# Performance work log

Measured on AMD Instinct MI355X. Metric: run time of the kernel, lower is better.

## Reference

```python
import math
import jax, jax.numpy as jnp
import numpy as np

B, S, D, H = 2, 2048, 1024, 16
HD = D // H  # head_dim = 64


def setup_inputs() -> dict:
    key = jax.random.key(0)
    k1, k2, k3 = jax.random.split(key, 3)
    scale = 0.02
    return {
        "x": jax.random.normal(k1, (B, S, D), dtype=jnp.float32),
        "w_qkv": jax.random.normal(k2, (D, 3 * D), dtype=jnp.float32) * scale,
        "b_qkv": jnp.zeros((3 * D,), dtype=jnp.float32),
        "w_proj": jax.random.normal(k3, (D, D), dtype=jnp.float32) * scale,
        "b_proj": jnp.zeros((D,), dtype=jnp.float32),
    }


def reference(x, w_qkv, b_qkv, w_proj, b_proj):
    bsz, seq_len, d_model = x.shape
    # fused qkv projection: [B,S,3D] -> [3,B,H,S,HD]
    qkv = (x @ w_qkv + b_qkv).reshape(bsz, seq_len, 3, H, HD)
    qkv = jnp.transpose(qkv, (2, 0, 3, 1, 4))
    q, k, v = qkv[0], qkv[1], qkv[2]
    # scores [B,H,S,S]
    scores = jnp.einsum("bhqd,bhkd->bhqk", q, k) / math.sqrt(HD)
    causal = jnp.tril(jnp.ones((seq_len, seq_len), dtype=bool))
    scores = jnp.where(causal[None, None], scores, -jnp.inf)
    probs = jax.nn.softmax(scores, axis=-1)
    # dropout = 0.0 (eval mode)
    context = jnp.einsum("bhqk,bhkd->bhqd", probs, v)
    context = jnp.transpose(context, (0, 2, 1, 3)).reshape(bsz, seq_len, d_model)
    return context @ w_proj + b_proj
```

## Files before the change

kernel.cpp:

```cpp
#include <hip/hip_runtime.h>

#define B_ 2
#define S_ 2048
#define D_ 1024
#define H_ 16
#define HD_ 64
#define M_ (B_*S_)
#define N_QKV (3*D_)

typedef __attribute__((ext_vector_type(8))) short short8;
typedef __attribute__((ext_vector_type(4))) float floatx4;

__device__ __forceinline__ float fast_exp2(float x) {
    return __builtin_amdgcn_exp2f(x);
}

__device__ __forceinline__ unsigned short f2b(float f) {
    union { float f; unsigned int u; } v; v.f = f;
    unsigned int u = v.u;
    u += 0x7FFFu + ((u >> 16) & 1u);
    return (unsigned short)(u >> 16);
}
__device__ __forceinline__ unsigned short f2b_fast(float f) {
    union { float f; unsigned int u; } v; v.f = f;
    return (unsigned short)((v.u + 0x8000u) >> 16);
}

__device__ __forceinline__ void glds16(const unsigned short* g, unsigned short* lds) {
    __builtin_amdgcn_global_load_lds(
        (const __attribute__((address_space(1))) unsigned int*)g,
        (__attribute__((address_space(3))) unsigned int*)lds, 16, 0, 0);
}

__global__ void cast_bf16_kernel(const float* __restrict__ src,
                                 unsigned short* __restrict__ dst, int n) {
    int i = (blockIdx.x * blockDim.x + threadIdx.x) * 4;
    if (i >= n) return;
    float4 f = *(const float4*)(src + i);
    ushort4 o;
    o.x = f2b(f.x); o.y = f2b(f.y); o.z = f2b(f.z); o.w = f2b(f.w);
    *(ushort4*)(dst + i) = o;
}

__global__ void transpose_cast_kernel(const float* __restrict__ W,
                                      unsigned short* __restrict__ Wt,
                                      int rows, int cols) {
    __shared__ float tile[32][33];
    int c0 = blockIdx.x * 32, r0 = blockIdx.y * 32;
    int tx = threadIdx.x, ty = threadIdx.y;
    #pragma unroll
    for (int i = 0; i < 4; ++i)
        tile[ty + i*8][tx] = W[(size_t)(r0 + ty + i*8) * cols + c0 + tx];
    __syncthreads();
    #pragma unroll
    for (int i = 0; i < 4; ++i)
        Wt[(size_t)(c0 + ty + i*8) * rows + r0 + tx] = f2b(tile[tx][ty + i*8]);
}

__global__ __launch_bounds__(256, 3) void gemm_bt_kernel(
    const unsigned short* __restrict__ A,
    const unsigned short* __restrict__ Bt,
    const float* __restrict__ bias,
    unsigned short* __restrict__ q,
    unsigned short* __restrict__ k_,
    unsigned short* __restrict__ vt,
    int Kdim)
{
    __shared__ unsigned short SMEM[128*136];
    unsigned short* As = SMEM;
    unsigned short* Bs = SMEM + 128*64;

    const int t = threadIdx.x;
    const int lane = t & 63;
    const int w = t >> 6;
    const int wm = w >> 1, wn = w & 1;
    const int quad = lane >> 4, l15 = lane & 15;
    const int bm = blockIdx.y, bn = blockIdx.x;

    const int sr32 = t >> 3;
    const int gch  = (t & 7) ^ (sr32 & 7);

    const unsigned short* gA = A  + (size_t)(bm*128 + sr32) * Kdim + gch*8;
    const unsigned short* gB = Bt + (size_t)(bn*128 + sr32) * Kdim + gch*8;
    const size_t rstep = (size_t)32 * Kdim;

    unsigned short* lA = As + (w*8)*64;
    unsigned short* lB = Bs + (w*8)*64;

    const int swz = (l15 & 7);

    auto stage_g = [&](int kk) {
        #pragma unroll
        for (int c = 0; c < 4; ++c) {
            glds16(gA + c*rstep + kk, lA + c*2048);
            glds16(gB + c*rstep + kk, lB + c*2048);
        }
    };

    floatx4 acc[4][4];
    #pragma unroll
    for (int i = 0; i < 4; ++i)
        #pragma unroll
        for (int j = 0; j < 4; ++j)
            acc[i][j] = (floatx4){0.f, 0.f, 0.f, 0.f};

    stage_g(0);
    for (int k0 = 0; k0 < Kdim; k0 += 64) {
        __syncthreads();
        short8 an[4][2], am[4][2];
        #pragma unroll
        for (int i = 0; i < 4; ++i)
            #pragma unroll
            for (int kk = 0; kk < 2; ++kk) {
                const int coff = ((quad + 4*kk) ^ swz) * 8;
                an[i][kk] = *(const short8*)&Bs[(wn*64 + i*16 + l15)*64 + coff];
                am[i][kk] = *(const short8*)&As[(wm*64 + i*16 + l15)*64 + coff];
            }
        __syncthreads();
        if (k0 + 64 < Kdim) stage_g(k0 + 64);
        #pragma unroll
        for (int kk = 0; kk < 2; ++kk)
            #pragma unroll
            for (int i = 0; i < 4; ++i)
                #pragma unroll
                for (int j = 0; j < 4; ++j)
                    acc[i][j] = __builtin_amdgcn_mfma_f32_16x16x32_bf16(an[i][kk], am[j][kk], acc[i][j], 0, 0, 0);
    }

    const float QSCALE = 0.18033688011112042f;
    const int which = bn >> 3;
    const int hcol  = (bn & 7)*2 + wn;
    const int b     = bm >> 4;
    const int sbase0 = (bm & 15)*128;
    const int sbase  = sbase0 + wm*64;

    if (which == 2) {
        unsigned short (*L)[136] = (unsigned short (*)[136])SMEM;
        #pragma unroll
        for (int i = 0; i < 4; ++i) {
            float4 bias4 = *(const float4*)&bias[bn*128 + wn*64 + i*16 + quad*4];
            const int n0 = wn*64 + i*16 + quad*4;
            #pragma unroll
            for (int j = 0; j < 4; ++j) {
                const int m = wm*64 + j*16 + l15;
                L[n0+0][m] = f2b(acc[i][j][0] + bias4.x);
                L[n0+1][m] = f2b(acc[i][j][1] + bias4.y);
                L[n0+2][m] = f2b(acc[i][j][2] + bias4.z);
                L[n0+3][m] = f2b(acc[i][j][3] + bias4.w);
            }
        }
        __syncthreads();
        const int r = t >> 1, half = t & 1;
        const int hcr = (bn & 7)*2 + (r >> 6);
        const int hdr = r & 63;
        unsigned short* dst = &vt[(((size_t)(b*H_ + hcr))*HD_ + hdr)*S_ + sbase0 + half*64];
        const unsigned short* srcL = &L[r][half*64];
        #pragma unroll
        for (int c = 0; c < 8; ++c)
            *(uint4*)&dst[c*8] = *(const uint4*)&srcL[c*8];
    } else {
        #pragma unroll
        for (int i = 0; i < 4; ++i) {
            float4 bias4 = *(const float4*)&bias[bn*128 + wn*64 + i*16 + quad*4];
            const int hd0 = i*16 + quad*4;
            #pragma unroll
            for (int j = 0; j < 4; ++j) {
                const int srow = sbase + j*16 + l15;
                float v0 = acc[i][j][0] + bias4.x;
                float v1 = acc[i][j][1] + bias4.y;
                float v2 = acc[i][j][2] + bias4.z;
                float v3 = acc[i][j][3] + bias4.w;
                if (which == 0) {
                    v0 *= QSCALE; v1 *= QSCALE; v2 *= QSCALE; v3 *= QSCALE;
                    ushort4 o; o.x = f2b(v0); o.y = f2b(v1); o.z = f2b(v2); o.w = f2b(v3);
                    *(ushort4*)&q[((size_t)(b*H_ + hcol) * S_ + srow) * HD_ + hd0] = o;
                } else {
                    ushort4 o; o.x = f2b(v0); o.y = f2b(v1); o.z = f2b(v2); o.w = f2b(v3);
                    *(ushort4*)&k_[((size_t)(b*H_ + hcol) * S_ + srow) * HD_ + hd0] = o;
                }
            }
        }
    }
}

__global__ __launch_bounds__(256, 2) void gemm_bt64_kernel(
    const unsigned short* __restrict__ A,
    const unsigned short* __restrict__ Bt,
    const float* __restrict__ bias,
    float* __restrict__ outf,
    int Ndim, int Kdim)
{
    __shared__ unsigned short As[128*64];
    __shared__ unsigned short Bs[64*64];

    const int t = threadIdx.x;
    const int lane = t & 63;
    const int w = t >> 6;
    const int quad = lane >> 4, l15 = lane & 15;
    const int bm = blockIdx.y, bn = blockIdx.x;

    const int sr32 = t >> 3;
    const int gch  = (t & 7) ^ (sr32 & 7);

    const unsigned short* gA = A  + (size_t)(bm*128 + sr32) * Kdim + gch*8;
    const unsigned short* gB = Bt + (size_t)(bn*64  + sr32) * Kdim + gch*8;
    const size_t rstep = (size_t)32 * Kdim;

    unsigned short* lA = As + (w*8)*64;
    unsigned short* lB = Bs + (w*8)*64;

    const int swz = (l15 & 7);

    auto stage_g = [&](int kk) {
        #pragma unroll
        for (int c = 0; c < 4; ++c)
            glds16(gA + c*rstep + kk, lA + c*2048);
        #pragma unroll
        for (int c = 0; c < 2; ++c)
            glds16(gB + c*rstep + kk, lB + c*2048);
    };

    floatx4 acc[4][2];
    #pragma unroll
    for (int i = 0; i < 4; ++i)
        #pragma unroll
        for (int j = 0; j < 2; ++j)
            acc[i][j] = (floatx4){0.f, 0.f, 0.f, 0.f};

    stage_g(0);
    for (int k0 = 0; k0 < Kdim; k0 += 64) {
        __syncthreads();
        short8 an[4][2], am[2][2];
        #pragma unroll
        for (int kk = 0; kk < 2; ++kk) {
            const int coff = ((quad + 4*kk) ^ swz) * 8;
            #pragma unroll
            for (int i = 0; i < 4; ++i)
                an[i][kk] = *(const short8*)&Bs[(i*16 + l15)*64 + coff];
            #pragma unroll
            for (int j = 0; j < 2; ++j)
                am[j][kk] = *(const short8*)&As[(w*32 + j*16 + l15)*64 + coff];
        }
        __syncthreads();
        if (k0 + 64 < Kdim) stage_g(k0 + 64);
        #pragma unroll
        for (int kk = 0; kk < 2; ++kk)
            #pragma unroll
            for (int i = 0; i < 4; ++i)
                #pragma unroll
                for (int j = 0; j < 2; ++j)
                    acc[i][j] = __builtin_amdgcn_mfma_f32_16x16x32_bf16(an[i][kk], am[j][kk], acc[i][j], 0, 0, 0);
    }

    #pragma unroll
    for (int i = 0; i < 4; ++i) {
        float4 bias4 = *(const float4*)&bias[bn*64 + i*16 + quad*4];
        #pragma unroll
        for (int j = 0; j < 2; ++j) {
            const int gm = bm*128 + w*32 + j*16 + l15;
            float4 o;
            o.x = acc[i][j][0] + bias4.x;
            o.y = acc[i][j][1] + bias4.y;
            o.z = acc[i][j][2] + bias4.z;
            o.w = acc[i][j][3] + bias4.w;
            *(float4*)&outf[(size_t)gm * Ndim + bn*64 + i*16 + quad*4] = o;
        }
    }
}

__global__ __launch_bounds__(256, 2) void attn_kernel(
    const unsigned short* __restrict__ Q,
    const unsigned short* __restrict__ K,
    const unsigned short* __restrict__ Vt,
    unsigned short* __restrict__ ctx)
{
    __shared__ unsigned short KVs[2][2][64*64];
    __shared__ unsigned short Pt[4][2][16][72];

    const int t = threadIdx.x;
    const int lane = t & 63, w = t >> 6;
    const int quad = lane >> 4, l15 = lane & 15;
    const int bh = blockIdx.x & 31;
    const int a  = blockIdx.x >> 5;
    const int Hc = 31 - a;
    const int Lc = a;

    const unsigned short* Qh  = Q  + (size_t)bh * S_ * HD_;
    const unsigned short* Kh  = K  + (size_t)bh * S_ * HD_;
    const unsigned short* Vth = Vt + (size_t)bh * HD_ * S_;

    const int sr = t >> 3, sc = t & 7;
    const int gch = sc ^ (sr & 7);

    auto stage = [&](int j, int d) {
        unsigned short* kb = &KVs[d][0][0];
        unsigned short* vb = &KVs[d][1][0];
        const unsigned short* gk = Kh  + (size_t)(j*64 + sr)*HD_ + gch*8;
        const unsigned short* gv = Vth + (size_t)sr*S_ + (size_t)j*64 + gch*8;
        glds16(gk,                  kb + (w*8)*64);
        glds16(gk + 32*HD_,         kb + (32 + w*8)*64);
        glds16(gv,                  vb + (w*8)*64);
        glds16(gv + (size_t)32*S_,  vb + (32 + w*8)*64);
    };

    const int qH = Hc*64 + w*16;
    const int qL = Lc*64 + w*16;

    short8 bqH[2], bqL[2];
    #pragma unroll
    for (int kk = 0; kk < 2; ++kk) {
        bqH[kk] = *(const short8*)&Qh[(size_t)(qH + l15)*HD_ + kk*32 + quad*8];
        bqL[kk] = *(const short8*)&Qh[(size_t)(qL + l15)*HD_ + kk*32 + quad*8];
    }

    floatx4 OH[4], OL[4];
    #pragma unroll
    for (int nb = 0; nb < 4; ++nb) {
        OH[nb] = (floatx4){0.f,0.f,0.f,0.f};
        OL[nb] = (floatx4){0.f,0.f,0.f,0.f};
    }
    float lH = 0.f, lL = 0.f;

    auto do_tile = [&](const short8 (&bq)[2], floatx4 (&O)[4], float& l_acc,
                       int qbase, bool diag, int j, int ps,
                       const short8 (&ak)[4][2], const short8 (&av)[4][2]) {
        float z[4][4];
        __builtin_amdgcn_s_setprio(1);
        #pragma unroll
        for (int nb = 0; nb < 4; ++nb) {
            floatx4 c = (floatx4){0.f,0.f,0.f,0.f};
            c = __builtin_amdgcn_mfma_f32_16x16x32_bf16(ak[nb][0], bq[0], c, 0,0,0);
            c = __builtin_amdgcn_mfma_f32_16x16x32_bf16(ak[nb][1], bq[1], c, 0,0,0);
            #pragma unroll
            for (int r = 0; r < 4; ++r) z[nb][r] = c[r];
        }
        __builtin_amdgcn_s_setprio(0);
        if (diag) {
            const int qg = qbase + l15, koff = j*64;
            #pragma unroll
            for (int nb = 0; nb < 4; ++nb)
                #pragma unroll
                for (int r = 0; r < 4; ++r)
                    if (koff + nb*16 + quad*4 + r > qg) z[nb][r] = -1e30f;
        }
        float rs = 0.f;
        #pragma unroll
        for (int nb = 0; nb < 4; ++nb) {
            float p0 = fast_exp2(z[nb][0]);
            float p1 = fast_exp2(z[nb][1]);
            float p2 = fast_exp2(z[nb][2]);
            float p3 = fast_exp2(z[nb][3]);
            rs += (p0 + p1) + (p2 + p3);
            ushort4 pk;
            pk.x = f2b_fast(p0); pk.y = f2b_fast(p1);
            pk.z = f2b_fast(p2); pk.w = f2b_fast(p3);
            *(ushort4*)&Pt[w][ps][l15][nb*16 + quad*4] = pk;
        }
        l_acc += rs;
        short8 bp0 = *(const short8*)&Pt[w][ps][l15][quad*8];
        short8 bp1 = *(const short8*)&Pt[w][ps][l15][32 + quad*8];
        __builtin_amdgcn_s_setprio(1);
        #pragma unroll
        for (int nb = 0; nb < 4; ++nb) {
            O[nb] = __builtin_amdgcn_mfma_f32_16x16x32_bf16(av[nb][0], bp0, O[nb], 0,0,0);
            O[nb] = __builtin_amdgcn_mfma_f32_16x16x32_bf16(av[nb][1], bp1, O[nb], 0,0,0);
        }
        __builtin_amdgcn_s_setprio(0);
    };

    stage(0, 0);

    for (int j = 0; j <= Hc; ++j) {
        __syncthreads();
        if (j < Hc) stage(j+1, (j+1)&1);
        const int d = j & 1;
        const unsigned short* Ksb = &KVs[d][0][0];
        const unsigned short* Vsb = &KVs[d][1][0];

        short8 ak[4][2], av[4][2];
        #pragma unroll
        for (int nb = 0; nb < 4; ++nb)
            #pragma unroll
            for (int kk = 0; kk < 2; ++kk) {
                int off = (nb*16 + l15)*64 + (((quad + 4*kk) ^ (l15 & 7)) * 8);
                ak[nb][kk] = *(const short8*)&Ksb[off];
                av[nb][kk] = *(const short8*)&Vsb[off];
            }

        do_tile(bqH, OH, lH, qH, j == Hc, j, 0, ak, av);
        if (j <= Lc)
            do_tile(bqL, OL, lL, qL, j == Lc, j, 1, ak, av);
    }

    const int b = bh >> 4, h = bh & (H_ - 1);
    auto finish = [&](floatx4 (&O)[4], float l_acc, int qbase) {
        l_acc += __shfl_xor(l_acc, 16, 64);
        l_acc += __shfl_xor(l_acc, 32, 64);
        const float inv = 1.f / l_acc;
        const int qg = qbase + l15;
        #pragma unroll
        for (int nb = 0; nb < 4; ++nb) {
            ushort4 o;
            o.x = f2b(O[nb][0] * inv);
            o.y = f2b(O[nb][1] * inv);
            o.z = f2b(O[nb][2] * inv);
            o.w = f2b(O[nb][3] * inv);
            *(ushort4*)&ctx[((size_t)(b*S_ + qg))*D_ + h*HD_ + nb*16 + quad*4] = o;
        }
    };
    finish(OH, lH, qH);
    finish(OL, lL, qL);
}

extern "C" void kernel_launch(void* const* d_in, const int* in_sizes, int n_in,
                              void* d_out, int out_size, void* d_ws, size_t ws_size,
                              hipStream_t stream) {
    const float* x      = (const float*)d_in[0];
    const float* w_qkv  = (const float*)d_in[1];
    const float* b_qkv  = (const float*)d_in[2];
    const float* w_proj = (const float*)d_in[3];
    const float* b_proj = (const float*)d_in[4];
    float* out = (float*)d_out;

    unsigned short* xb     = (unsigned short*)d_ws;
    unsigned short* wqkvT  = xb     + (size_t)M_ * D_;
    unsigned short* wprojT = wqkvT  + (size_t)N_QKV * D_;
    unsigned short* Qb     = wprojT + (size_t)D_ * D_;
    unsigned short* Kb     = Qb     + (size_t)B_*H_*S_*HD_;
    unsigned short* Vb     = Kb     + (size_t)B_*H_*S_*HD_;
    unsigned short* Vtb    = Vb     + (size_t)B_*H_*S_*HD_;
    unsigned short* ctx    = xb;

    cast_bf16_kernel<<<dim3((M_*D_/4 + 255)/256), dim3(256), 0, stream>>>(x, xb, M_*D_);
    transpose_cast_kernel<<<dim3(N_QKV/32, D_/32), dim3(32, 8), 0, stream>>>(w_qkv, wqkvT, D_, N_QKV);
    transpose_cast_kernel<<<dim3(D_/32, D_/32), dim3(32, 8), 0, stream>>>(w_proj, wprojT, D_, D_);

    gemm_bt_kernel<<<dim3(N_QKV/128, M_/128), dim3(256), 0, stream>>>(
        xb, wqkvT, b_qkv, Qb, Kb, Vtb, D_);

    attn_kernel<<<dim3(512), dim3(256), 0, stream>>>(Qb, Kb, Vtb, ctx);

    gemm_bt64_kernel<<<dim3(D_/64, M_/128), dim3(256), 0, stream>>>(
        ctx, wprojT, b_proj, out, D_, D_);
}
```

Baseline: 172.3 us.

## Load K and V tiles directly from global memory into registers, dropping LDS staging

Removes the shared-memory double-buffered K/V staging (async global-to-LDS copies plus a block barrier per tile). Each wave now loads its K fragments straight from global memory into registers with a two-buffer software prefetch, and loads V fragments directly inside the compute step. This eliminates the __syncthreads and LDS traffic, at the cost of every wave fetching the same K/V data separately. That duplicates global/L2 traffic fourfold, raises register pressure, and leaves the V loads unprefetched.

```diff
diff --git a/kernel.cpp b/kernel.cpp
--- a/kernel.cpp
+++ b/kernel.cpp
@@ -274,7 +274,6 @@
     const unsigned short* __restrict__ Vt,
     unsigned short* __restrict__ ctx)
 {
-    __shared__ unsigned short KVs[2][2][64*64];
     __shared__ unsigned short Pt[4][2][16][72];
 
     const int t = threadIdx.x;
@@ -289,20 +288,6 @@
     const unsigned short* Kh  = K  + (size_t)bh * S_ * HD_;
     const unsigned short* Vth = Vt + (size_t)bh * HD_ * S_;
 
-    const int sr = t >> 3, sc = t & 7;
-    const int gch = sc ^ (sr & 7);
-
-    auto stage = [&](int j, int d) {
-        unsigned short* kb = &KVs[d][0][0];
-        unsigned short* vb = &KVs[d][1][0];
-        const unsigned short* gk = Kh  + (size_t)(j*64 + sr)*HD_ + gch*8;
-        const unsigned short* gv = Vth + (size_t)sr*S_ + (size_t)j*64 + gch*8;
-        glds16(gk,                  kb + (w*8)*64);
-        glds16(gk + 32*HD_,         kb + (32 + w*8)*64);
-        glds16(gv,                  vb + (w*8)*64);
-        glds16(gv + (size_t)32*S_,  vb + (32 + w*8)*64);
-    };
-
     const int qH = Hc*64 + w*16;
     const int qL = Lc*64 + w*16;
 
@@ -320,6 +305,14 @@
         OL[nb] = (floatx4){0.f,0.f,0.f,0.f};
     }
     float lH = 0.f, lL = 0.f;
+
+    auto load_k = [&](int j, short8 (&ak)[4][2]) {
+        #pragma unroll
+        for (int nb = 0; nb < 4; ++nb)
+            #pragma unroll
+            for (int kk = 0; kk < 2; ++kk)
+                ak[nb][kk] = *(const short8*)&Kh[(size_t)(j*64 + nb*16 + l15)*HD_ + (quad + 4*kk)*8];
+    };
 
     auto do_tile = [&](const short8 (&bq)[2], floatx4 (&O)[4], float& l_acc,
                        int qbase, bool diag, int j, int ps,
@@ -368,28 +361,30 @@
         __builtin_amdgcn_s_setprio(0);
     };
 
-    stage(0, 0);
-
-    for (int j = 0; j <= Hc; ++j) {
-        __syncthreads();
-        if (j < Hc) stage(j+1, (j+1)&1);
-        const int d = j & 1;
-        const unsigned short* Ksb = &KVs[d][0][0];
-        const unsigned short* Vsb = &KVs[d][1][0];
-
-        short8 ak[4][2], av[4][2];
+    auto compute = [&](int j, const short8 (&ak)[4][2]) {
+        short8 av[4][2];
         #pragma unroll
         for (int nb = 0; nb < 4; ++nb)
             #pragma unroll
-            for (int kk = 0; kk < 2; ++kk) {
-                int off = (nb*16 + l15)*64 + (((quad + 4*kk) ^ (l15 & 7)) * 8);
-                ak[nb][kk] = *(const short8*)&Ksb[off];
-                av[nb][kk] = *(const short8*)&Vsb[off];
-            }
-
+            for (int kk = 0; kk < 2; ++kk)
+                av[nb][kk] = *(const short8*)&Vth[(size_t)(nb*16 + l15)*S_ + j*64 + (quad + 4*kk)*8];
         do_tile(bqH, OH, lH, qH, j == Hc, j, 0, ak, av);
         if (j <= Lc)
             do_tile(bqL, OL, lL, qL, j == Lc, j, 1, ak, av);
+    };
+
+    short8 akA[4][2], akB[4][2];
+    load_k(0, akA);
+    int j = 0;
+    for (;;) {
+        if (j < Hc) load_k(j + 1, akB);
+        compute(j, akA);
+        if (j == Hc) break;
+        ++j;
+        if (j < Hc) load_k(j + 1, akA);
+        compute(j, akB);
+        if (j == Hc) break;
+        ++j;
     }
 
     const int b = bh >> 4, h = bh & (H_ - 1);
```

Result: slower. 235.3 us (+36.6%).

## Split paired-chunk attention blocks into single-chunk blocks and fuse prep kernels

Applied to the files above, without the earlier changes.

The attention kernel no longer pairs a high and a low causal query chunk in each block. It launches 1024 blocks, each handling one 64-row query chunk, ordered longest-first within each head, with occupancy raised to 3 blocks per CU through smaller P scratch and fewer registers. This drops the K/V tile sharing between the two chunks, so K/V traffic roughly doubles, in exchange for more parallel work and occupancy. Separately, the x cast and the two weight transpose-casts are merged into one prep kernel launch to cut launch overhead.

```diff
diff --git a/kernel.cpp b/kernel.cpp
--- a/kernel.cpp
+++ b/kernel.cpp
@@ -32,29 +32,39 @@
         (__attribute__((address_space(3))) unsigned int*)lds, 16, 0, 0);
 }
 
-__global__ void cast_bf16_kernel(const float* __restrict__ src,
-                                 unsigned short* __restrict__ dst, int n) {
-    int i = (blockIdx.x * blockDim.x + threadIdx.x) * 4;
-    if (i >= n) return;
-    float4 f = *(const float4*)(src + i);
-    ushort4 o;
-    o.x = f2b(f.x); o.y = f2b(f.y); o.z = f2b(f.z); o.w = f2b(f.w);
-    *(ushort4*)(dst + i) = o;
-}
-
-__global__ void transpose_cast_kernel(const float* __restrict__ W,
-                                      unsigned short* __restrict__ Wt,
-                                      int rows, int cols) {
+__global__ __launch_bounds__(256) void prep_kernel(
+    const float* __restrict__ x,      unsigned short* __restrict__ xb,
+    const float* __restrict__ w_qkv,  unsigned short* __restrict__ wqkvT,
+    const float* __restrict__ w_proj, unsigned short* __restrict__ wprojT)
+{
     __shared__ float tile[32][33];
-    int c0 = blockIdx.x * 32, r0 = blockIdx.y * 32;
-    int tx = threadIdx.x, ty = threadIdx.y;
-    #pragma unroll
-    for (int i = 0; i < 4; ++i)
-        tile[ty + i*8][tx] = W[(size_t)(r0 + ty + i*8) * cols + c0 + tx];
-    __syncthreads();
-    #pragma unroll
-    for (int i = 0; i < 4; ++i)
-        Wt[(size_t)(c0 + ty + i*8) * rows + r0 + tx] = f2b(tile[tx][ty + i*8]);
+    const int id = blockIdx.x;
+    if (id < 4096) {
+        const int i = (id * 256 + threadIdx.x) * 4;
+        float4 f = *(const float4*)(x + i);
+        ushort4 o;
+        o.x = f2b(f.x); o.y = f2b(f.y); o.z = f2b(f.z); o.w = f2b(f.w);
+        *(ushort4*)(xb + i) = o;
+    } else {
+        const float* W; unsigned short* Wt; int cols, bx, by;
+        if (id < 4096 + 3072) {
+            W = w_qkv; Wt = wqkvT; cols = N_QKV;
+            const int r = id - 4096; bx = r % 96; by = r / 96;
+        } else {
+            W = w_proj; Wt = wprojT; cols = D_;
+            const int r = id - 7168; bx = r % 32; by = r / 32;
+        }
+        const int rows = D_;
+        const int tx = threadIdx.x & 31, ty = threadIdx.x >> 5;
+        const int c0 = bx * 32, r0 = by * 32;
+        #pragma unroll
+        for (int i = 0; i < 4; ++i)
+            tile[ty + i*8][tx] = W[(size_t)(r0 + ty + i*8) * cols + c0 + tx];
+        __syncthreads();
+        #pragma unroll
+        for (int i = 0; i < 4; ++i)
+            Wt[(size_t)(c0 + ty + i*8) * rows + r0 + tx] = f2b(tile[tx][ty + i*8]);
+    }
 }
 
 __global__ __launch_bounds__(256, 3) void gemm_bt_kernel(
@@ -268,22 +278,20 @@
     }
 }
 
-__global__ __launch_bounds__(256, 2) void attn_kernel(
+__global__ __launch_bounds__(256, 3) void attn_kernel(
     const unsigned short* __restrict__ Q,
     const unsigned short* __restrict__ K,
     const unsigned short* __restrict__ Vt,
     unsigned short* __restrict__ ctx)
 {
     __shared__ unsigned short KVs[2][2][64*64];
-    __shared__ unsigned short Pt[4][2][16][72];
+    __shared__ unsigned short Pt[4][16][72];
 
     const int t = threadIdx.x;
     const int lane = t & 63, w = t >> 6;
     const int quad = lane >> 4, l15 = lane & 15;
-    const int bh = blockIdx.x & 31;
-    const int a  = blockIdx.x >> 5;
-    const int Hc = 31 - a;
-    const int Lc = a;
+    const int bh = blockIdx.x >> 5;
+    const int c  = 31 - (blockIdx.x & 31);
 
     const unsigned short* Qh  = Q  + (size_t)bh * S_ * HD_;
     const unsigned short* Kh  = K  + (size_t)bh * S_ * HD_;
@@ -303,46 +311,59 @@
         glds16(gv + (size_t)32*S_,  vb + (32 + w*8)*64);
     };
 
-    const int qH = Hc*64 + w*16;
-    const int qL = Lc*64 + w*16;
-
-    short8 bqH[2], bqL[2];
-    #pragma unroll
-    for (int kk = 0; kk < 2; ++kk) {
-        bqH[kk] = *(const short8*)&Qh[(size_t)(qH + l15)*HD_ + kk*32 + quad*8];
-        bqL[kk] = *(const short8*)&Qh[(size_t)(qL + l15)*HD_ + kk*32 + quad*8];
-    }
-
-    floatx4 OH[4], OL[4];
-    #pragma unroll
-    for (int nb = 0; nb < 4; ++nb) {
-        OH[nb] = (floatx4){0.f,0.f,0.f,0.f};
-        OL[nb] = (floatx4){0.f,0.f,0.f,0.f};
-    }
-    float lH = 0.f, lL = 0.f;
-
-    auto do_tile = [&](const short8 (&bq)[2], floatx4 (&O)[4], float& l_acc,
-                       int qbase, bool diag, int j, int ps,
-                       const short8 (&ak)[4][2], const short8 (&av)[4][2]) {
+    const int qc = c*64 + w*16;
+
+    short8 bq[2];
+    #pragma unroll
+    for (int kk = 0; kk < 2; ++kk)
+        bq[kk] = *(const short8*)&Qh[(size_t)(qc + l15)*HD_ + kk*32 + quad*8];
+
+    floatx4 O[4];
+    #pragma unroll
+    for (int nb = 0; nb < 4; ++nb)
+        O[nb] = (floatx4){0.f,0.f,0.f,0.f};
+    float l_acc = 0.f;
+
+    stage(0, 0);
+
+    for (int j = 0; j <= c; ++j) {
+        __syncthreads();
+        if (j < c) stage(j+1, (j+1)&1);
+        const int d = j & 1;
+        const unsigned short* Ksb = &KVs[d][0][0];
+        const unsigned short* Vsb = &KVs[d][1][0];
+
+        short8 ak[4][2], av[4][2];
+        #pragma unroll
+        for (int nb = 0; nb < 4; ++nb)
+            #pragma unroll
+            for (int kk = 0; kk < 2; ++kk) {
+                int off = (nb*16 + l15)*64 + (((quad + 4*kk) ^ (l15 & 7)) * 8);
+                ak[nb][kk] = *(const short8*)&Ksb[off];
+                av[nb][kk] = *(const short8*)&Vsb[off];
+            }
+
         float z[4][4];
         __builtin_amdgcn_s_setprio(1);
         #pragma unroll
         for (int nb = 0; nb < 4; ++nb) {
-            floatx4 c = (floatx4){0.f,0.f,0.f,0.f};
-            c = __builtin_amdgcn_mfma_f32_16x16x32_bf16(ak[nb][0], bq[0], c, 0,0,0);
-            c = __builtin_amdgcn_mfma_f32_16x16x32_bf16(ak[nb][1], bq[1], c, 0,0,0);
-            #pragma unroll
-            for (int r = 0; r < 4; ++r) z[nb][r] = c[r];
+            floatx4 cc = (floatx4){0.f,0.f,0.f,0.f};
+            cc = __builtin_amdgcn_mfma_f32_16x16x32_bf16(ak[nb][0], bq[0], cc, 0,0,0);
+            cc = __builtin_amdgcn_mfma_f32_16x16x32_bf16(ak[nb][1], bq[1], cc, 0,0,0);
+            #pragma unroll
+            for (int r = 0; r < 4; ++r) z[nb][r] = cc[r];
         }
         __builtin_amdgcn_s_setprio(0);
-        if (diag) {
-            const int qg = qbase + l15, koff = j*64;
+
+        if (j == c) {
+            const int qg = qc + l15, koff = j*64;
             #pragma unroll
             for (int nb = 0; nb < 4; ++nb)
                 #pragma unroll
                 for (int r = 0; r < 4; ++r)
                     if (koff + nb*16 + quad*4 + r > qg) z[nb][r] = -1e30f;
         }
+
         float rs = 0.f;
         #pragma unroll
         for (int nb = 0; nb < 4; ++nb) {
@@ -354,11 +375,12 @@
             ushort4 pk;
             pk.x = f2b_fast(p0); pk.y = f2b_fast(p1);
             pk.z = f2b_fast(p2); pk.w = f2b_fast(p3);
-            *(ushort4*)&Pt[w][ps][l15][nb*16 + quad*4] = pk;
+            *(ushort4*)&Pt[w][l15][nb*16 + quad*4] = pk;
         }
         l_acc += rs;
-        short8 bp0 = *(const short8*)&Pt[w][ps][l15][quad*8];
-        short8 bp1 = *(const short8*)&Pt[w][ps][l15][32 + quad*8];
+
+        short8 bp0 = *(const short8*)&Pt[w][l15][quad*8];
+        short8 bp1 = *(const short8*)&Pt[w][l15][32 + quad*8];
         __builtin_amdgcn_s_setprio(1);
         #pragma unroll
         for (int nb = 0; nb < 4; ++nb) {
@@ -366,50 +388,22 @@
             O[nb] = __builtin_amdgcn_mfma_f32_16x16x32_bf16(av[nb][1], bp1, O[nb], 0,0,0);
         }
         __builtin_amdgcn_s_setprio(0);
-    };
-
-    stage(0, 0);
-
-    for (int j = 0; j <= Hc; ++j) {
-        __syncthreads();
-        if (j < Hc) stage(j+1, (j+1)&1);
-        const int d = j & 1;
-        const unsigned short* Ksb = &KVs[d][0][0];
-        const unsigned short* Vsb = &KVs[d][1][0];
-
-        short8 ak[4][2], av[4][2];
-        #pragma unroll
-        for (int nb = 0; nb < 4; ++nb)
-            #pragma unroll
-            for (int kk = 0; kk < 2; ++kk) {
-                int off = (nb*16 + l15)*64 + (((quad + 4*kk) ^ (l15 & 7)) * 8);
-                ak[nb][kk] = *(const short8*)&Ksb[off];
-                av[nb][kk] = *(const short8*)&Vsb[off];
-            }
-
-        do_tile(bqH, OH, lH, qH, j == Hc, j, 0, ak, av);
-        if (j <= Lc)
-            do_tile(bqL, OL, lL, qL, j == Lc, j, 1, ak, av);
     }
 
     const int b = bh >> 4, h = bh & (H_ - 1);
-    auto finish = [&](floatx4 (&O)[4], float l_acc, int qbase) {
-        l_acc += __shfl_xor(l_acc, 16, 64);
-        l_acc += __shfl_xor(l_acc, 32, 64);
-        const float inv = 1.f / l_acc;
-        const int qg = qbase + l15;
-        #pragma unroll
-        for (int nb = 0; nb < 4; ++nb) {
-            ushort4 o;
-            o.x = f2b(O[nb][0] * inv);
-            o.y = f2b(O[nb][1] * inv);
-            o.z = f2b(O[nb][2] * inv);
-            o.w = f2b(O[nb][3] * inv);
-            *(ushort4*)&ctx[((size_t)(b*S_ + qg))*D_ + h*HD_ + nb*16 + quad*4] = o;
-        }
-    };
-    finish(OH, lH, qH);
-    finish(OL, lL, qL);
+    l_acc += __shfl_xor(l_acc, 16, 64);
+    l_acc += __shfl_xor(l_acc, 32, 64);
+    const float inv = 1.f / l_acc;
+    const int qg = qc + l15;
+    #pragma unroll
+    for (int nb = 0; nb < 4; ++nb) {
+        ushort4 o;
+        o.x = f2b(O[nb][0] * inv);
+        o.y = f2b(O[nb][1] * inv);
+        o.z = f2b(O[nb][2] * inv);
+        o.w = f2b(O[nb][3] * inv);
+        *(ushort4*)&ctx[((size_t)(b*S_ + qg))*D_ + h*HD_ + nb*16 + quad*4] = o;
+    }
 }
 
 extern "C" void kernel_launch(void* const* d_in, const int* in_sizes, int n_in,
@@ -431,14 +425,12 @@
     unsigned short* Vtb    = Vb     + (size_t)B_*H_*S_*HD_;
     unsigned short* ctx    = xb;
 
-    cast_bf16_kernel<<<dim3((M_*D_/4 + 255)/256), dim3(256), 0, stream>>>(x, xb, M_*D_);
-    transpose_cast_kernel<<<dim3(N_QKV/32, D_/32), dim3(32, 8), 0, stream>>>(w_qkv, wqkvT, D_, N_QKV);
-    transpose_cast_kernel<<<dim3(D_/32, D_/32), dim3(32, 8), 0, stream>>>(w_proj, wprojT, D_, D_);
+    prep_kernel<<<dim3(8192), dim3(256), 0, stream>>>(x, xb, w_qkv, wqkvT, w_proj, wprojT);
 
     gemm_bt_kernel<<<dim3(N_QKV/128, M_/128), dim3(256), 0, stream>>>(
         xb, wqkvT, b_qkv, Qb, Kb, Vtb, D_);
 
-    attn_kernel<<<dim3(512), dim3(256), 0, stream>>>(Qb, Kb, Vtb, ctx);
+    attn_kernel<<<dim3(1024), dim3(256), 0, stream>>>(Qb, Kb, Vtb, ctx);
 
     gemm_bt64_kernel<<<dim3(D_/64, M_/128), dim3(256), 0, stream>>>(
         ctx, wprojT, b_proj, out, D_, D_);
```

Measured after the change: 195.5 us. +13.5%, slower.
